# Performance work log

Hardware: AMD Instinct MI355X
Metric: run time of the kernel (lower is better)

Reference implementation:

```python
import jax, jax.numpy as jnp
import numpy as np

PATCH = 5
DIM = 256
HEADS = 8
EPS = 1e-5


def split_patches(t, p):
    # t: [B,H,W,C] -> overlapping patches [B,H,W,p,p,C], stride 1, zero-pad p//2
    pad = p // 2
    tp = jnp.pad(t, ((0, 0), (pad, pad), (pad, pad), (0, 0)))
    H, W = t.shape[1], t.shape[2]
    rows = jnp.arange(H)[:, None] + jnp.arange(p)[None, :]  # [H,p]
    cols = jnp.arange(W)[:, None] + jnp.arange(p)[None, :]  # [W,p]
    return tp[:, rows[:, None, :, None], cols[None, :, None, :], :]


def layernorm(v, g, b):
    mu = jnp.mean(v, axis=-1, keepdims=True)
    var = jnp.var(v, axis=-1, keepdims=True)
    return (v - mu) * jax.lax.rsqrt(var + EPS) * g + b


def mha(q, k, v, w, b, mask):
    # w: [4,D,D] stacked (Wq,Wk,Wv,Wo), b: [4,D]; q:[N,Lq,D], k,v:[N,Lk,D]
    N, Lq, D = q.shape
    dh = D // HEADS
    qh = (q @ w[0] + b[0]).reshape(N, Lq, HEADS, dh)
    kh = (k @ w[1] + b[1]).reshape(N, -1, HEADS, dh)
    vh = (v @ w[2] + b[2]).reshape(N, -1, HEADS, dh)
    sc = jnp.einsum('nqhd,nkhd->nhqk', qh, kh) * (1.0 / float(np.sqrt(dh)))
    if mask is not None:
        sc = jnp.where(mask, sc, jnp.asarray(-1e9, sc.dtype))
    a = jax.nn.softmax(sc, axis=-1)
    o = jnp.einsum('nhqk,nkhd->nqhd', a, vh).reshape(N, Lq, D)
    return o @ w[3] + b[3], a


def setup_inputs() -> dict:
    key = jax.random.key(0)
    ks = jax.random.split(key, 10)
    B, H, W, D = 1, 64, 64, DIM
    x = jax.random.normal(ks[0], (B, H, W, D), dtype=jnp.float32)
    memory = jax.random.normal(ks[1], (B, H, W, D), dtype=jnp.float32)
    active_nodes = jax.random.randint(ks[2], (B, H, W), 0, 2).astype(bool)
    s = 0.05
    return {
        'x': x, 'memory': memory, 'active_nodes': active_nodes,
        'attn_w': jax.random.normal(ks[3], (4, D, D), dtype=jnp.float32) * s,
        'attn_b': jnp.zeros((4, D), dtype=jnp.float32),
        'pattn_w': jax.random.normal(ks[4], (4, D, D), dtype=jnp.float32) * s,
        'pattn_b': jnp.zeros((4, D), dtype=jnp.float32),
        'ff_w1': jax.random.normal(ks[5], (D, 2 * D), dtype=jnp.float32) * s,
        'ff_b1': jnp.zeros((2 * D,), dtype=jnp.float32),
        'ff_w2': jax.random.normal(ks[6], (2 * D, D), dtype=jnp.float32) * s,
        'ff_b2': jnp.zeros((D,), dtype=jnp.float32),
        'ln_g': jnp.ones((3, D), dtype=jnp.float32),   # norm1, norm2, norm3
        'ln_b': jnp.zeros((3, D), dtype=jnp.float32),
    }


def reference(x, memory, active_nodes, attn_w, attn_b, pattn_w, pattn_b,
              ff_w1, ff_b1, ff_w2, ff_b2, ln_g, ln_b):
    B, H, W, D = x.shape
    p = PATCH
    center = p // 2
    L = p * p
    cp = L // 2  # flattened center point

    act = active_nodes[..., None]                      # [B,H,W,1] bool
    ap = split_patches(act, p)                         # [B,H,W,p,p,1]
    # faithful to source: zeroes the entire patch at GRID position (center,center)
    ap = ap.at[:, center, center].set(False)
    wo_center = jnp.any(ap.reshape(B, H, W, L, 1), axis=3)  # [B,H,W,1]
    act = jnp.logical_and(wo_center, act)
    ap = split_patches(act, p)                         # recomputed with updated mask

    xp = split_patches(x, p) * ap                      # zero inactive neighbors
    xp = xp.reshape(B, H, W, L, D)
    mp = split_patches(memory, p).reshape(B, H, W, L, D)
    mask = ap[..., 0].reshape(B, H, W, L)

    N = B * H * W
    keys = xp.reshape(N, L, D)
    mem = mp.reshape(N, L, D)
    q = keys[:, cp:cp + 1, :]                          # [N,1,D]
    m = mask.reshape(N, L)[:, None, None, :]           # [N,1,1,L]

    # EncoderLayer (eval mode: dropout = identity)
    s_, attn = mha(q, keys, keys, attn_w, attn_b, m)
    s = layernorm(q + s_, ln_g[0], ln_b[0])            # norm1
    s_, _ = mha(s, mem, mem, pattn_w, pattn_b, None)
    s = layernorm(s + s_, ln_g[2], ln_b[2])            # norm3
    ff = jax.nn.relu(s @ ff_w1 + ff_b1) @ ff_w2 + ff_b2
    s = layernorm(s + ff, ln_g[1], ln_b[1])            # norm2

    out = jnp.where(act, s[:, 0, :].reshape(B, H, W, D), jnp.asarray(0.0, x.dtype))
    return out, act[..., 0]
```

## Files before the change

kernel.cpp:

```cpp
#include <hip/hip_runtime.h>
#include <math.h>

#define D 256
#define H2 512
#define HEADS 8
#define L 25
#define GH 64
#define GW 64
#define NN 4096
#define EPS 1e-5f
#define SCALE 0.17677669529663687f
#define NND 1048576

typedef __attribute__((ext_vector_type(8))) short short8;
typedef __attribute__((ext_vector_type(4))) float f32x4;

__device__ __forceinline__ bool act_at(const int* __restrict__ active, int h, int w) {
    if (h < 0 || h >= GH || w < 0 || w >= GW) return false;
    if (h == 2 && w == 2) return false;
    return active[h * GW + w] != 0;
}

__device__ __forceinline__ unsigned short f2b(float f) {
    unsigned u = __float_as_uint(f);
    u += 0x7fffu + ((u >> 16) & 1u);
    return (unsigned short)(u >> 16);
}
__device__ __forceinline__ float b2f(short v) {
    return __uint_as_float(((unsigned)(unsigned short)v) << 16);
}

__global__ __launch_bounds__(256)
void prep_kernel(const float* __restrict__ x, const float* __restrict__ mem,
                 const int* __restrict__ active,
                 const float* __restrict__ attn_w, const float* __restrict__ pattn_w,
                 const float* __restrict__ ff_w1, const float* __restrict__ ff_w2,
                 const float* __restrict__ pattn_b,
                 unsigned short* __restrict__ xmB, unsigned short* __restrict__ memB,
                 unsigned short* __restrict__ wB,
                 unsigned short* __restrict__ k2bias, unsigned short* __restrict__ v2bias) {
    const int tid = threadIdx.x;
    const int bid = blockIdx.x;
    if (bid < 192) {
        __shared__ float tile[64][65];
        const float* src; unsigned short* dst;
        int i0, n0, srcLen, dstLen;
        if (bid < 128) {
            int mat = bid >> 4, t16 = bid & 15;
            i0 = (t16 >> 2) * 64; n0 = (t16 & 3) * 64;
            src = (mat < 4) ? (attn_w + mat * 65536) : (pattn_w + (mat - 4) * 65536);
            dst = wB + mat * 65536;
            srcLen = 256; dstLen = 256;
        } else if (bid < 160) {
            int t = bid - 128;
            i0 = (t >> 3) * 64; n0 = (t & 7) * 64;
            src = ff_w1; dst = wB + 524288;
            srcLen = 512; dstLen = 256;
        } else {
            int t = bid - 160;
            i0 = (t >> 2) * 64; n0 = (t & 3) * 64;
            src = ff_w2; dst = wB + 655360;
            srcLen = 256; dstLen = 512;
        }
        int c = tid & 63, r4 = tid >> 6;
        for (int rr = 0; rr < 64; rr += 4)
            tile[rr + r4][c] = src[(size_t)(i0 + rr + r4) * srcLen + n0 + c];
        __syncthreads();
        for (int rr = 0; rr < 64; rr += 4) {
            int r = rr + r4;
            dst[(size_t)(n0 + r) * dstLen + i0 + c] = f2b(tile[c][r]);
        }
    } else {
        const int t0 = (bid - 192) * 256 + tid;
        for (int t = t0; t < 524800; t += 512 * 256) {
            if (t < 262144) {
                int n = t >> 6;
                bool a = act_at(active, n >> 6, n & 63);
                float4 v = ((const float4*)x)[t];
                ushort4 u;
                u.x = f2b(a ? v.x : 0.0f); u.y = f2b(a ? v.y : 0.0f);
                u.z = f2b(a ? v.z : 0.0f); u.w = f2b(a ? v.w : 0.0f);
                ((ushort4*)xmB)[t] = u;
            } else if (t < 524288) {
                int tt = t - 262144;
                float4 v = ((const float4*)mem)[tt];
                ushort4 u;
                u.x = f2b(v.x); u.y = f2b(v.y); u.z = f2b(v.z); u.w = f2b(v.w);
                ((ushort4*)memB)[tt] = u;
            } else {
                int tt = t - 524288;
                if (tt < 256) k2bias[tt] = f2b(pattn_b[256 + tt]);
                else          v2bias[tt - 256] = f2b(pattn_b[512 + (tt - 256)]);
            }
        }
    }
}

__global__ __launch_bounds__(256)
void proj_gemm(const unsigned short* __restrict__ xmB,
               const unsigned short* __restrict__ memB,
               const unsigned short* __restrict__ wB,
               const float* __restrict__ attn_b, const float* __restrict__ pattn_b,
               unsigned short* __restrict__ q1b, unsigned short* __restrict__ k1b,
               unsigned short* __restrict__ v1b, unsigned short* __restrict__ k2b,
               unsigned short* __restrict__ v2b) {
    const int s  = blockIdx.y >> 2;
    const int n0 = (blockIdx.y & 3) * 64;
    const unsigned short* A  = (s < 3) ? xmB : memB;
    const int wtIdx = (s < 3) ? s : (s + 2);
    const unsigned short* WT = wB + (size_t)wtIdx * 65536;
    const float* bias = (s < 3) ? (attn_b + s * 256) : (pattn_b + (s - 2) * 256);
    unsigned short* outB;
    switch (s) { case 0: outB = q1b; break; case 1: outB = k1b; break;
                 case 2: outB = v1b; break; case 3: outB = k2b; break;
                 default: outB = v2b; }

    const int tid = threadIdx.x;
    const int wave = tid >> 6, lane = tid & 63;
    const int m0 = blockIdx.x * 64 + wave * 16;
    const int lr = lane & 15;
    const int lk = (lane >> 4) << 3;
    f32x4 acc[4] = {};
    const unsigned short* arow = A  + (size_t)(m0 + lr) * 256 + lk;
    const unsigned short* brow = WT + (size_t)(n0 + lr) * 256 + lk;
    #pragma unroll
    for (int kk = 0; kk < 256; kk += 32) {
        short8 a = *(const short8*)(arow + kk);
        #pragma unroll
        for (int nf = 0; nf < 4; ++nf) {
            short8 b = *(const short8*)(brow + (size_t)nf * 16 * 256 + kk);
            acc[nf] = __builtin_amdgcn_mfma_f32_16x16x32_bf16(a, b, acc[nf], 0, 0, 0);
        }
    }
    const int rbase = m0 + ((lane >> 4) << 2);
    #pragma unroll
    for (int nf = 0; nf < 4; ++nf) {
        int c = n0 + nf * 16 + lr;
        float bc = bias[c];
        #pragma unroll
        for (int jj = 0; jj < 4; ++jj)
            outB[(size_t)(rbase + jj) * 256 + c] = f2b(acc[nf][jj] + bc);
    }
}

#define KV_OFF   0
#define ACT_OFF  51200
#define WGT_OFF  51328
#define REDA_OFF 64128
#define REDB_OFF 64640
#define STAT_OFF 65152
#define SMEM_SZ  65280
#define T1B_OFF  0
#define SB_OFF   8448
#define HB_OFF   16896

__device__ __forceinline__ void load_union(const unsigned short* __restrict__ base,
                                           int h, int w0, int fallback,
                                           unsigned short (*kvU)[256], int tid) {
    for (int c = tid; c < 3200; c += 512) {
        int u = c >> 5, part = c & 31;
        int r = u / 20;
        int hh = h - 2 + r, ww = w0 - 2 + (u - r * 20);
        bool ib = ((unsigned)hh < GH) && ((unsigned)ww < GW);
        int row = ib ? ((hh << 6) | ww) : fallback;
        *(uint4*)&kvU[u][part * 8] = *(const uint4*)(base + (size_t)row * 256 + part * 8);
    }
}

__global__ __launch_bounds__(512)
void fused_kernel(const int* __restrict__ active, const float* __restrict__ x,
                  const unsigned short* __restrict__ wB,
                  const float* __restrict__ attn_b, const float* __restrict__ pattn_b,
                  const float* __restrict__ ff_b1, const float* __restrict__ ff_b2,
                  const float* __restrict__ ln_g, const float* __restrict__ ln_b,
                  const unsigned short* __restrict__ q1b,
                  const unsigned short* __restrict__ k1b,
                  const unsigned short* __restrict__ v1b,
                  const unsigned short* __restrict__ k2b,
                  const unsigned short* __restrict__ v2b,
                  float* __restrict__ out) {
    const int tid = threadIdx.x;
    const int wv = tid >> 6, lane = tid & 63;
    const int lr = lane & 15, qi = lane >> 4;
    const int bid = ((blockIdx.x & 7) << 5) | (blockIdx.x >> 3);
    const int n0 = bid * 16;
    const int h = n0 >> 6, w0 = n0 & 63;
    const int half = lane >> 5, lam = lane & 31;
    const int m = wv * 2 + half;

    __shared__ __align__(16) char smem[SMEM_SZ];
    unsigned short (*kvU)[256] = (unsigned short(*)[256])(smem + KV_OFF);
    unsigned char* actU        = (unsigned char*)(smem + ACT_OFF);
    float (*wgt)[8][25]        = (float(*)[8][25])(smem + WGT_OFF);
    float (*redA)[8]           = (float(*)[8])(smem + REDA_OFF);
    float (*redB)[8]           = (float(*)[8])(smem + REDB_OFF);
    float (*stats)[2]          = (float(*)[2])(smem + STAT_OFF);
    unsigned short (*T1b)[264] = (unsigned short(*)[264])(smem + T1B_OFF);
    unsigned short (*Sb)[264]  = (unsigned short(*)[264])(smem + SB_OFF);
    unsigned short (*Hb)[520]  = (unsigned short(*)[520])(smem + HB_OFF);

    if (tid < 100) {
        int r = tid / 20;
        int hh = h - 2 + r, ww = w0 - 2 + (tid - r * 20);
        actU[tid] = act_at(active, hh, ww) ? 1 : 0;
    }
    load_union(k1b, h, w0, 0, kvU, tid);
    __syncthreads();

    {
        float q[8];
        short8 qv = *(const short8*)(q1b + (size_t)(n0 + m) * 256 + lam * 8);
        #pragma unroll
        for (int j = 0; j < 8; ++j) q[j] = b2f(qv[j]);
        #pragma unroll 5
        for (int l = 0; l < L; ++l) {
            int u = (l / 5) * 20 + m + (l % 5);
            short8 kv = *(const short8*)&kvU[u][lam * 8];
            float p = q[0] * b2f(kv[0]);
            #pragma unroll
            for (int j = 1; j < 8; ++j) p = fmaf(q[j], b2f(kv[j]), p);
            p += __shfl_xor(p, 1); p += __shfl_xor(p, 2);
            float sv = actU[u] ? p * SCALE : -1e30f;
            if ((lam & 3) == 0) wgt[m][lam >> 2][l] = sv;
        }
    }
    __syncthreads();
    if (tid < 128) {
        int mm = tid >> 3, hd = tid & 7;
        float mx = -1e30f;
        for (int l = 0; l < L; ++l) mx = fmaxf(mx, wgt[mm][hd][l]);
        float sum = 0.0f;
        for (int l = 0; l < L; ++l) { float e = expf(wgt[mm][hd][l] - mx); wgt[mm][hd][l] = e; sum += e; }
        float inv = 1.0f / sum;
        for (int l = 0; l < L; ++l) wgt[mm][hd][l] *= inv;
    }
    __syncthreads();
    load_union(v1b, h, w0, 0, kvU, tid);
    __syncthreads();
    {
        float o[8] = {0.f,0.f,0.f,0.f,0.f,0.f,0.f,0.f};
        #pragma unroll 5
        for (int l = 0; l < L; ++l) {
            int u = (l / 5) * 20 + m + (l % 5);
            if (actU[u]) {
                float wt = wgt[m][lam >> 2][l];
                short8 v8 = *(const short8*)&kvU[u][lam * 8];
                #pragma unroll
                for (int j = 0; j < 8; ++j) o[j] = fmaf(wt, b2f(v8[j]), o[j]);
            }
        }
        __syncthreads();
        unsigned short u8[8];
        #pragma unroll
        for (int j = 0; j < 8; ++j) u8[j] = f2b(o[j]);
        *(uint4*)&T1b[m][lam * 8] = *(uint4*)u8;
    }
    __syncthreads();

    float sreg[2][4];
    {
        const unsigned short* Wo1T = wB + 3 * 65536;
        f32x4 acc[2] = {};
        #pragma unroll
        for (int kk = 0; kk < 256; kk += 32) {
            short8 a = *(const short8*)&T1b[lr][qi * 8 + kk];
            #pragma unroll
            for (int nf = 0; nf < 2; ++nf) {
                short8 b = *(const short8*)(Wo1T + (size_t)(wv * 32 + nf * 16 + lr) * 256 + qi * 8 + kk);
                acc[nf] = __builtin_amdgcn_mfma_f32_16x16x32_bf16(a, b, acc[nf], 0, 0, 0);
            }
        }
        float v[2][4], s1[4] = {0.f,0.f,0.f,0.f}, s2[4] = {0.f,0.f,0.f,0.f};
        #pragma unroll
        for (int nf = 0; nf < 2; ++nf) {
            int c = wv * 32 + nf * 16 + lr;
            float bc = attn_b[768 + c];
            #pragma unroll
            for (int jj = 0; jj < 4; ++jj) {
                int row = n0 + qi * 4 + jj;
                float vv = acc[nf][jj] + bc + x[(size_t)row * D + c];
                v[nf][jj] = vv; s1[jj] += vv; s2[jj] += vv * vv;
            }
        }
        #pragma unroll
        for (int jj = 0; jj < 4; ++jj) {
            #pragma unroll
            for (int off = 1; off < 16; off <<= 1) {
                s1[jj] += __shfl_xor(s1[jj], off);
                s2[jj] += __shfl_xor(s2[jj], off);
            }
        }
        if (lr == 0) {
            #pragma unroll
            for (int jj = 0; jj < 4; ++jj) { redA[qi*4+jj][wv] = s1[jj]; redB[qi*4+jj][wv] = s2[jj]; }
        }
        __syncthreads();
        if (tid < 16) {
            float a1 = 0.f, a2 = 0.f;
            #pragma unroll
            for (int q8 = 0; q8 < 8; ++q8) { a1 += redA[tid][q8]; a2 += redB[tid][q8]; }
            float mu = a1 * (1.0f / D);
            float var = a2 * (1.0f / D) - mu * mu;
            stats[tid][0] = mu; stats[tid][1] = rsqrtf(var + EPS);
        }
        __syncthreads();
        #pragma unroll
        for (int nf = 0; nf < 2; ++nf) {
            int c = wv * 32 + nf * 16 + lr;
            float gg = ln_g[c], bb = ln_b[c];
            #pragma unroll
            for (int jj = 0; jj < 4; ++jj) {
                int ridx = qi * 4 + jj;
                float ov = (v[nf][jj] - stats[ridx][0]) * stats[ridx][1] * gg + bb;
                sreg[nf][jj] = ov;
                Sb[ridx][c] = f2b(ov);
            }
        }
    }
    __syncthreads();

    {
        const unsigned short* Wq2T = wB + 4 * 65536;
        f32x4 acc[2] = {};
        #pragma unroll
        for (int kk = 0; kk < 256; kk += 32) {
            short8 a = *(const short8*)&Sb[lr][qi * 8 + kk];
            #pragma unroll
            for (int nf = 0; nf < 2; ++nf) {
                short8 b = *(const short8*)(Wq2T + (size_t)(wv * 32 + nf * 16 + lr) * 256 + qi * 8 + kk);
                acc[nf] = __builtin_amdgcn_mfma_f32_16x16x32_bf16(a, b, acc[nf], 0, 0, 0);
            }
        }
        __syncthreads();
        #pragma unroll
        for (int nf = 0; nf < 2; ++nf) {
            int c = wv * 32 + nf * 16 + lr;
            float bc = pattn_b[c];
            #pragma unroll
            for (int jj = 0; jj < 4; ++jj)
                T1b[qi * 4 + jj][c] = f2b(acc[nf][jj] + bc);
        }
    }
    __syncthreads();

    float q2[8];
    {
        short8 qv = *(const short8*)&T1b[m][lam * 8];
        #pragma unroll
        for (int j = 0; j < 8; ++j) q2[j] = b2f(qv[j]);
    }
    __syncthreads();
    load_union(k2b, h, w0, NN, kvU, tid);
    __syncthreads();

    #pragma unroll 5
    for (int l = 0; l < L; ++l) {
        int u = (l / 5) * 20 + m + (l % 5);
        short8 kv = *(const short8*)&kvU[u][lam * 8];
        float p = q2[0] * b2f(kv[0]);
        #pragma unroll
        for (int j = 1; j < 8; ++j) p = fmaf(q2[j], b2f(kv[j]), p);
        p += __shfl_xor(p, 1); p += __shfl_xor(p, 2);
        if ((lam & 3) == 0) wgt[m][lam >> 2][l] = p * SCALE;
    }
    __syncthreads();
    if (tid < 128) {
        int mm = tid >> 3, hd = tid & 7;
        float mx = -1e30f;
        for (int l = 0; l < L; ++l) mx = fmaxf(mx, wgt[mm][hd][l]);
        float sum = 0.0f;
        for (int l = 0; l < L; ++l) { float e = expf(wgt[mm][hd][l] - mx); wgt[mm][hd][l] = e; sum += e; }
        float inv = 1.0f / sum;
        for (int l = 0; l < L; ++l) wgt[mm][hd][l] *= inv;
    }
    __syncthreads();
    load_union(v2b, h, w0, NN, kvU, tid);
    __syncthreads();
    {
        float o[8] = {0.f,0.f,0.f,0.f,0.f,0.f,0.f,0.f};
        #pragma unroll 5
        for (int l = 0; l < L; ++l) {
            int u = (l / 5) * 20 + m + (l % 5);
            float wt = wgt[m][lam >> 2][l];
            short8 v8 = *(const short8*)&kvU[u][lam * 8];
            #pragma unroll
            for (int j = 0; j < 8; ++j) o[j] = fmaf(wt, b2f(v8[j]), o[j]);
        }
        __syncthreads();
        unsigned short u8[8];
        #pragma unroll
        for (int j = 0; j < 8; ++j) u8[j] = f2b(o[j]);
        *(uint4*)&T1b[m][lam * 8] = *(uint4*)u8;
    }
    __syncthreads();

    float s2reg[2][4];
    {
        const unsigned short* Wo2T = wB + 7 * 65536;
        f32x4 acc[2] = {};
        #pragma unroll
        for (int kk = 0; kk < 256; kk += 32) {
            short8 a = *(const short8*)&T1b[lr][qi * 8 + kk];
            #pragma unroll
            for (int nf = 0; nf < 2; ++nf) {
                short8 b = *(const short8*)(Wo2T + (size_t)(wv * 32 + nf * 16 + lr) * 256 + qi * 8 + kk);
                acc[nf] = __builtin_amdgcn_mfma_f32_16x16x32_bf16(a, b, acc[nf], 0, 0, 0);
            }
        }
        float v[2][4], s1[4] = {0.f,0.f,0.f,0.f}, s2[4] = {0.f,0.f,0.f,0.f};
        #pragma unroll
        for (int nf = 0; nf < 2; ++nf) {
            int c = wv * 32 + nf * 16 + lr;
            float bc = pattn_b[768 + c];
            #pragma unroll
            for (int jj = 0; jj < 4; ++jj) {
                float vv = acc[nf][jj] + bc + sreg[nf][jj];
                v[nf][jj] = vv; s1[jj] += vv; s2[jj] += vv * vv;
            }
        }
        #pragma unroll
        for (int jj = 0; jj < 4; ++jj) {
            #pragma unroll
            for (int off = 1; off < 16; off <<= 1) {
                s1[jj] += __shfl_xor(s1[jj], off);
                s2[jj] += __shfl_xor(s2[jj], off);
            }
        }
        if (lr == 0) {
            #pragma unroll
            for (int jj = 0; jj < 4; ++jj) { redA[qi*4+jj][wv] = s1[jj]; redB[qi*4+jj][wv] = s2[jj]; }
        }
        __syncthreads();
        if (tid < 16) {
            float a1 = 0.f, a2 = 0.f;
            #pragma unroll
            for (int q8 = 0; q8 < 8; ++q8) { a1 += redA[tid][q8]; a2 += redB[tid][q8]; }
            float mu = a1 * (1.0f / D);
            float var = a2 * (1.0f / D) - mu * mu;
            stats[tid][0] = mu; stats[tid][1] = rsqrtf(var + EPS);
        }
        __syncthreads();
        #pragma unroll
        for (int nf = 0; nf < 2; ++nf) {
            int c = wv * 32 + nf * 16 + lr;
            float gg = ln_g[512 + c], bb = ln_b[512 + c];
            #pragma unroll
            for (int jj = 0; jj < 4; ++jj) {
                int ridx = qi * 4 + jj;
                float ov = (v[nf][jj] - stats[ridx][0]) * stats[ridx][1] * gg + bb;
                s2reg[nf][jj] = ov;
                Sb[ridx][c] = f2b(ov);
            }
        }
    }
    __syncthreads();

    {
        const unsigned short* W1T = wB + 524288;
        f32x4 acc[4] = {};
        #pragma unroll
        for (int kk = 0; kk < 256; kk += 32) {
            short8 a = *(const short8*)&Sb[lr][qi * 8 + kk];
            #pragma unroll
            for (int nf = 0; nf < 4; ++nf) {
                short8 b = *(const short8*)(W1T + (size_t)(wv * 64 + nf * 16 + lr) * 256 + qi * 8 + kk);
                acc[nf] = __builtin_amdgcn_mfma_f32_16x16x32_bf16(a, b, acc[nf], 0, 0, 0);
            }
        }
        #pragma unroll
        for (int nf = 0; nf < 4; ++nf) {
            int c = wv * 64 + nf * 16 + lr;
            float bc = ff_b1[c];
            #pragma unroll
            for (int jj = 0; jj < 4; ++jj)
                Hb[qi * 4 + jj][c] = f2b(fmaxf(acc[nf][jj] + bc, 0.0f));
        }
    }
    __syncthreads();

    {
        const unsigned short* W2T = wB + 655360;
        f32x4 acc[2] = {};
        #pragma unroll
        for (int kk = 0; kk < 512; kk += 32) {
            short8 a = *(const short8*)&Hb[lr][qi * 8 + kk];
            #pragma unroll
            for (int nf = 0; nf < 2; ++nf) {
                short8 b = *(const short8*)(W2T + (size_t)(wv * 32 + nf * 16 + lr) * 512 + qi * 8 + kk);
                acc[nf] = __builtin_amdgcn_mfma_f32_16x16x32_bf16(a, b, acc[nf], 0, 0, 0);
            }
        }
        float v[2][4], s1[4] = {0.f,0.f,0.f,0.f}, s2[4] = {0.f,0.f,0.f,0.f};
        #pragma unroll
        for (int nf = 0; nf < 2; ++nf) {
            int c = wv * 32 + nf * 16 + lr;
            float bc = ff_b2[c];
            #pragma unroll
            for (int jj = 0; jj < 4; ++jj) {
                float vv = acc[nf][jj] + bc + s2reg[nf][jj];
                v[nf][jj] = vv; s1[jj] += vv; s2[jj] += vv * vv;
            }
        }
        #pragma unroll
        for (int jj = 0; jj < 4; ++jj) {
            #pragma unroll
            for (int off = 1; off < 16; off <<= 1) {
                s1[jj] += __shfl_xor(s1[jj], off);
                s2[jj] += __shfl_xor(s2[jj], off);
            }
        }
        if (lr == 0) {
            #pragma unroll
            for (int jj = 0; jj < 4; ++jj) { redA[qi*4+jj][wv] = s1[jj]; redB[qi*4+jj][wv] = s2[jj]; }
        }
        __syncthreads();
        if (tid < 16) {
            float a1 = 0.f, a2 = 0.f;
            #pragma unroll
            for (int q8 = 0; q8 < 8; ++q8) { a1 += redA[tid][q8]; a2 += redB[tid][q8]; }
            float mu = a1 * (1.0f / D);
            float var = a2 * (1.0f / D) - mu * mu;
            stats[tid][0] = mu; stats[tid][1] = rsqrtf(var + EPS);
        }
        __syncthreads();
        bool arow_act[4];
        #pragma unroll
        for (int jj = 0; jj < 4; ++jj) {
            int row = n0 + qi * 4 + jj;
            arow_act[jj] = act_at(active, row >> 6, row & 63);
        }
        #pragma unroll
        for (int nf = 0; nf < 2; ++nf) {
            int c = wv * 32 + nf * 16 + lr;
            float gg = ln_g[256 + c], bb = ln_b[256 + c];
            #pragma unroll
            for (int jj = 0; jj < 4; ++jj) {
                int ridx = qi * 4 + jj;
                float ov = (v[nf][jj] - stats[ridx][0]) * stats[ridx][1] * gg + bb;
                out[(size_t)(n0 + ridx) * D + c] = arow_act[jj] ? ov : 0.0f;
            }
        }
        if (tid < 16) {
            int row = n0 + tid;
            out[(size_t)NND + row] = act_at(active, row >> 6, row & 63) ? 1.0f : 0.0f;
        }
    }
}

extern "C" void kernel_launch(void* const* d_in, const int* in_sizes, int n_in,
                              void* d_out, int out_size, void* d_ws, size_t ws_size,
                              hipStream_t stream) {
    const float* x       = (const float*)d_in[0];
    const float* memory  = (const float*)d_in[1];
    const int*   active  = (const int*)d_in[2];
    const float* attn_w  = (const float*)d_in[3];
    const float* attn_b  = (const float*)d_in[4];
    const float* pattn_w = (const float*)d_in[5];
    const float* pattn_b = (const float*)d_in[6];
    const float* ff_w1   = (const float*)d_in[7];
    const float* ff_b1   = (const float*)d_in[8];
    const float* ff_w2   = (const float*)d_in[9];
    const float* ff_b2   = (const float*)d_in[10];
    const float* ln_g    = (const float*)d_in[11];
    const float* ln_b    = (const float*)d_in[12];
    float* out = (float*)d_out;

    unsigned short* wsb = (unsigned short*)d_ws;
    unsigned short* xmB  = wsb;
    unsigned short* memB = wsb + (size_t)NND;
    unsigned short* wB   = wsb + 2 * (size_t)NND;
    unsigned short* q1b  = wB + 786432;
    unsigned short* k1b  = q1b + (size_t)NND;
    unsigned short* v1b  = k1b + (size_t)NND;
    unsigned short* k2b  = v1b + (size_t)NND;
    unsigned short* v2b  = k2b + (size_t)NND + 256;

    hipLaunchKernelGGL(prep_kernel, dim3(704), dim3(256), 0, stream,
                       x, memory, active, attn_w, pattn_w, ff_w1, ff_w2, pattn_b,
                       xmB, memB, wB, k2b + (size_t)NND, v2b + (size_t)NND);
    hipLaunchKernelGGL(proj_gemm, dim3(64, 20), dim3(256), 0, stream,
                       xmB, memB, wB, attn_b, pattn_b, q1b, k1b, v1b, k2b, v2b);
    hipLaunchKernelGGL(fused_kernel, dim3(256), dim3(512), 0, stream,
                       active, x, wB, attn_b, pattn_b, ff_b1, ff_b2, ln_g, ln_b,
                       q1b, k1b, v1b, k2b, v2b, out);
}
```

Before: 91.11 us.

## Fuse input bf16 conversion into projection GEMM and double-buffer neighbor K/V loads

The prep kernel no longer converts x and memory to bf16 buffers. The projection GEMM now reads fp32 inputs directly, applies the active mask and converts in registers, which removes a full write and re-read of two activation tensors. The fused kernel now uses separate K and V LDS buffers in a larger dynamic shared allocation. It prefetches the next stage's K2/V2 union into registers while softmax and attention compute run, cutting several serialized global-load barriers. The trade-off is more LDS per block, about 150KB, and more registers. The GEMM also reads fp32 A twice from global, which is more traffic per tile than bf16.

```diff
diff --git a/kernel.cpp b/kernel.cpp
--- a/kernel.cpp
+++ b/kernel.cpp
@@ -31,12 +31,9 @@
 }
 
 __global__ __launch_bounds__(256)
-void prep_kernel(const float* __restrict__ x, const float* __restrict__ mem,
-                 const int* __restrict__ active,
-                 const float* __restrict__ attn_w, const float* __restrict__ pattn_w,
+void prep_kernel(const float* __restrict__ attn_w, const float* __restrict__ pattn_w,
                  const float* __restrict__ ff_w1, const float* __restrict__ ff_w2,
                  const float* __restrict__ pattn_b,
-                 unsigned short* __restrict__ xmB, unsigned short* __restrict__ memB,
                  unsigned short* __restrict__ wB,
                  unsigned short* __restrict__ k2bias, unsigned short* __restrict__ v2bias) {
     const int tid = threadIdx.x;
@@ -71,34 +68,16 @@
             dst[(size_t)(n0 + r) * dstLen + i0 + c] = f2b(tile[c][r]);
         }
     } else {
-        const int t0 = (bid - 192) * 256 + tid;
-        for (int t = t0; t < 524800; t += 512 * 256) {
-            if (t < 262144) {
-                int n = t >> 6;
-                bool a = act_at(active, n >> 6, n & 63);
-                float4 v = ((const float4*)x)[t];
-                ushort4 u;
-                u.x = f2b(a ? v.x : 0.0f); u.y = f2b(a ? v.y : 0.0f);
-                u.z = f2b(a ? v.z : 0.0f); u.w = f2b(a ? v.w : 0.0f);
-                ((ushort4*)xmB)[t] = u;
-            } else if (t < 524288) {
-                int tt = t - 262144;
-                float4 v = ((const float4*)mem)[tt];
-                ushort4 u;
-                u.x = f2b(v.x); u.y = f2b(v.y); u.z = f2b(v.z); u.w = f2b(v.w);
-                ((ushort4*)memB)[tt] = u;
-            } else {
-                int tt = t - 524288;
-                if (tt < 256) k2bias[tt] = f2b(pattn_b[256 + tt]);
-                else          v2bias[tt - 256] = f2b(pattn_b[512 + (tt - 256)]);
-            }
+        if (tid < 256) {
+            k2bias[tid] = f2b(pattn_b[256 + tid]);
+            v2bias[tid] = f2b(pattn_b[512 + tid]);
         }
     }
 }
 
 __global__ __launch_bounds__(256)
-void proj_gemm(const unsigned short* __restrict__ xmB,
-               const unsigned short* __restrict__ memB,
+void proj_gemm(const float* __restrict__ x, const float* __restrict__ mem,
+               const int* __restrict__ active,
                const unsigned short* __restrict__ wB,
                const float* __restrict__ attn_b, const float* __restrict__ pattn_b,
                unsigned short* __restrict__ q1b, unsigned short* __restrict__ k1b,
@@ -106,7 +85,8 @@
                unsigned short* __restrict__ v2b) {
     const int s  = blockIdx.y >> 2;
     const int n0 = (blockIdx.y & 3) * 64;
-    const unsigned short* A  = (s < 3) ? xmB : memB;
+    const float* Asrc = (s < 3) ? x : mem;
+    const bool useMask = (s < 3);
     const int wtIdx = (s < 3) ? s : (s + 2);
     const unsigned short* WT = wB + (size_t)wtIdx * 65536;
     const float* bias = (s < 3) ? (attn_b + s * 256) : (pattn_b + (s - 2) * 256);
@@ -120,12 +100,25 @@
     const int m0 = blockIdx.x * 64 + wave * 16;
     const int lr = lane & 15;
     const int lk = (lane >> 4) << 3;
+    const int arowIdx = m0 + lr;
+    const bool rowAct = !useMask || act_at(active, arowIdx >> 6, arowIdx & 63);
+
     f32x4 acc[4] = {};
-    const unsigned short* arow = A  + (size_t)(m0 + lr) * 256 + lk;
+    const float* arow = Asrc + (size_t)arowIdx * 256 + lk;
     const unsigned short* brow = WT + (size_t)(n0 + lr) * 256 + lk;
     #pragma unroll
     for (int kk = 0; kk < 256; kk += 32) {
-        short8 a = *(const short8*)(arow + kk);
+        float4 a0 = *(const float4*)(arow + kk);
+        float4 a1 = *(const float4*)(arow + kk + 4);
+        short8 a;
+        a[0] = rowAct ? (short)f2b(a0.x) : (short)0;
+        a[1] = rowAct ? (short)f2b(a0.y) : (short)0;
+        a[2] = rowAct ? (short)f2b(a0.z) : (short)0;
+        a[3] = rowAct ? (short)f2b(a0.w) : (short)0;
+        a[4] = rowAct ? (short)f2b(a1.x) : (short)0;
+        a[5] = rowAct ? (short)f2b(a1.y) : (short)0;
+        a[6] = rowAct ? (short)f2b(a1.z) : (short)0;
+        a[7] = rowAct ? (short)f2b(a1.w) : (short)0;
         #pragma unroll
         for (int nf = 0; nf < 4; ++nf) {
             short8 b = *(const short8*)(brow + (size_t)nf * 16 * 256 + kk);
@@ -143,27 +136,33 @@
     }
 }
 
-#define KV_OFF   0
-#define ACT_OFF  51200
-#define WGT_OFF  51328
-#define REDA_OFF 64128
-#define REDB_OFF 64640
-#define STAT_OFF 65152
-#define SMEM_SZ  65280
-#define T1B_OFF  0
-#define SB_OFF   8448
-#define HB_OFF   16896
-
-__device__ __forceinline__ void load_union(const unsigned short* __restrict__ base,
-                                           int h, int w0, int fallback,
-                                           unsigned short (*kvU)[256], int tid) {
+#define BK_OFF   0
+#define BV_OFF   51200
+#define WGT_OFF  102400
+#define T1B_OFF  115200
+#define SB_OFF   123648
+#define HB_OFF   132096
+#define ACT_OFF  148736
+#define REDA_OFF 148864
+#define REDB_OFF 149376
+#define STAT_OFF 149888
+#define SMEM_SZ  150016
+
+__device__ __forceinline__ int union_row(int c, int h, int w0, int fallback) {
+    int u = c >> 5;
+    int r = u / 20;
+    int hh = h - 2 + r, ww = w0 - 2 + (u - r * 20);
+    bool ib = ((unsigned)hh < GH) && ((unsigned)ww < GW);
+    return ib ? ((hh << 6) | ww) : fallback;
+}
+
+__device__ __forceinline__ void load_union_lds(const unsigned short* __restrict__ base,
+                                               int h, int w0, int fallback,
+                                               unsigned short (*dst)[256], int tid) {
     for (int c = tid; c < 3200; c += 512) {
+        int row = union_row(c, h, w0, fallback);
         int u = c >> 5, part = c & 31;
-        int r = u / 20;
-        int hh = h - 2 + r, ww = w0 - 2 + (u - r * 20);
-        bool ib = ((unsigned)hh < GH) && ((unsigned)ww < GW);
-        int row = ib ? ((hh << 6) | ww) : fallback;
-        *(uint4*)&kvU[u][part * 8] = *(const uint4*)(base + (size_t)row * 256 + part * 8);
+        *(uint4*)&dst[u][part * 8] = *(const uint4*)(base + (size_t)row * 256 + part * 8);
     }
 }
 
@@ -179,32 +178,34 @@
                   const unsigned short* __restrict__ k2b,
                   const unsigned short* __restrict__ v2b,
                   float* __restrict__ out) {
+    extern __shared__ __align__(16) char smem[];
+    unsigned short (*bufK)[256] = (unsigned short(*)[256])(smem + BK_OFF);
+    unsigned short (*bufV)[256] = (unsigned short(*)[256])(smem + BV_OFF);
+    float (*wgt)[8][25]         = (float(*)[8][25])(smem + WGT_OFF);
+    unsigned short (*T1b)[264]  = (unsigned short(*)[264])(smem + T1B_OFF);
+    unsigned short (*Sb)[264]   = (unsigned short(*)[264])(smem + SB_OFF);
+    unsigned short (*Hb)[520]   = (unsigned short(*)[520])(smem + HB_OFF);
+    unsigned char* actU         = (unsigned char*)(smem + ACT_OFF);
+    float (*redA)[8]            = (float(*)[8])(smem + REDA_OFF);
+    float (*redB)[8]            = (float(*)[8])(smem + REDB_OFF);
+    float (*stats)[2]           = (float(*)[2])(smem + STAT_OFF);
+
     const int tid = threadIdx.x;
     const int wv = tid >> 6, lane = tid & 63;
     const int lr = lane & 15, qi = lane >> 4;
+    const int half = lane >> 5, lam = lane & 31;
+    const int m = wv * 2 + half;
     const int bid = ((blockIdx.x & 7) << 5) | (blockIdx.x >> 3);
     const int n0 = bid * 16;
     const int h = n0 >> 6, w0 = n0 & 63;
-    const int half = lane >> 5, lam = lane & 31;
-    const int m = wv * 2 + half;
-
-    __shared__ __align__(16) char smem[SMEM_SZ];
-    unsigned short (*kvU)[256] = (unsigned short(*)[256])(smem + KV_OFF);
-    unsigned char* actU        = (unsigned char*)(smem + ACT_OFF);
-    float (*wgt)[8][25]        = (float(*)[8][25])(smem + WGT_OFF);
-    float (*redA)[8]           = (float(*)[8])(smem + REDA_OFF);
-    float (*redB)[8]           = (float(*)[8])(smem + REDB_OFF);
-    float (*stats)[2]          = (float(*)[2])(smem + STAT_OFF);
-    unsigned short (*T1b)[264] = (unsigned short(*)[264])(smem + T1B_OFF);
-    unsigned short (*Sb)[264]  = (unsigned short(*)[264])(smem + SB_OFF);
-    unsigned short (*Hb)[520]  = (unsigned short(*)[520])(smem + HB_OFF);
 
     if (tid < 100) {
         int r = tid / 20;
         int hh = h - 2 + r, ww = w0 - 2 + (tid - r * 20);
         actU[tid] = act_at(active, hh, ww) ? 1 : 0;
     }
-    load_union(k1b, h, w0, 0, kvU, tid);
+    load_union_lds(k1b, h, w0, 0, bufK, tid);
+    load_union_lds(v1b, h, w0, 0, bufV, tid);
     __syncthreads();
 
     {
@@ -215,7 +216,7 @@
         #pragma unroll 5
         for (int l = 0; l < L; ++l) {
             int u = (l / 5) * 20 + m + (l % 5);
-            short8 kv = *(const short8*)&kvU[u][lam * 8];
+            short8 kv = *(const short8*)&bufK[u][lam * 8];
             float p = q[0] * b2f(kv[0]);
             #pragma unroll
             for (int j = 1; j < 8; ++j) p = fmaf(q[j], b2f(kv[j]), p);
@@ -223,6 +224,167 @@
             float sv = actU[u] ? p * SCALE : -1e30f;
             if ((lam & 3) == 0) wgt[m][lam >> 2][l] = sv;
         }
+    }
+    __syncthreads();
+
+    uint4 pre[7];
+    {
+        #pragma unroll
+        for (int k = 0; k < 7; ++k) {
+            int c = tid + k * 512;
+            int cc = (c < 3200) ? c : 3199;
+            int row = union_row(cc, h, w0, NN);
+            pre[k] = *(const uint4*)(k2b + (size_t)row * 256 + (cc & 31) * 8);
+        }
+        if (tid < 128) {
+            int mm = tid >> 3, hd = tid & 7;
+            float mx = -1e30f;
+            for (int l = 0; l < L; ++l) mx = fmaxf(mx, wgt[mm][hd][l]);
+            float sum = 0.0f;
+            for (int l = 0; l < L; ++l) { float e = expf(wgt[mm][hd][l] - mx); wgt[mm][hd][l] = e; sum += e; }
+            float inv = 1.0f / sum;
+            for (int l = 0; l < L; ++l) wgt[mm][hd][l] *= inv;
+        }
+        #pragma unroll
+        for (int k = 0; k < 7; ++k) {
+            int c = tid + k * 512;
+            if (c < 3200)
+                *(uint4*)&bufK[c >> 5][(c & 31) * 8] = pre[k];
+        }
+    }
+    __syncthreads();
+
+    {
+        #pragma unroll
+        for (int k = 0; k < 7; ++k) {
+            int c = tid + k * 512;
+            int cc = (c < 3200) ? c : 3199;
+            int row = union_row(cc, h, w0, NN);
+            pre[k] = *(const uint4*)(v2b + (size_t)row * 256 + (cc & 31) * 8);
+        }
+        float o[8] = {0.f,0.f,0.f,0.f,0.f,0.f,0.f,0.f};
+        #pragma unroll 5
+        for (int l = 0; l < L; ++l) {
+            int u = (l / 5) * 20 + m + (l % 5);
+            if (actU[u]) {
+                float wt = wgt[m][lam >> 2][l];
+                short8 v8 = *(const short8*)&bufV[u][lam * 8];
+                #pragma unroll
+                for (int j = 0; j < 8; ++j) o[j] = fmaf(wt, b2f(v8[j]), o[j]);
+            }
+        }
+        unsigned short u8[8];
+        #pragma unroll
+        for (int j = 0; j < 8; ++j) u8[j] = f2b(o[j]);
+        *(uint4*)&T1b[m][lam * 8] = *(uint4*)u8;
+    }
+    __syncthreads();
+
+    float sreg[2][4];
+    {
+        #pragma unroll
+        for (int k = 0; k < 7; ++k) {
+            int c = tid + k * 512;
+            if (c < 3200)
+                *(uint4*)&bufV[c >> 5][(c & 31) * 8] = pre[k];
+        }
+        const unsigned short* Wo1T = wB + 3 * 65536;
+        f32x4 acc[2] = {};
+        #pragma unroll
+        for (int kk = 0; kk < 256; kk += 32) {
+            short8 a = *(const short8*)&T1b[lr][qi * 8 + kk];
+            #pragma unroll
+            for (int nf = 0; nf < 2; ++nf) {
+                short8 b = *(const short8*)(Wo1T + (size_t)(wv * 32 + nf * 16 + lr) * 256 + qi * 8 + kk);
+                acc[nf] = __builtin_amdgcn_mfma_f32_16x16x32_bf16(a, b, acc[nf], 0, 0, 0);
+            }
+        }
+        float v[2][4], s1[4] = {0.f,0.f,0.f,0.f}, s2[4] = {0.f,0.f,0.f,0.f};
+        #pragma unroll
+        for (int nf = 0; nf < 2; ++nf) {
+            int c = wv * 32 + nf * 16 + lr;
+            float bc = attn_b[768 + c];
+            #pragma unroll
+            for (int jj = 0; jj < 4; ++jj) {
+                int row = n0 + qi * 4 + jj;
+                float vv = acc[nf][jj] + bc + x[(size_t)row * D + c];
+                v[nf][jj] = vv; s1[jj] += vv; s2[jj] += vv * vv;
+            }
+        }
+        #pragma unroll
+        for (int jj = 0; jj < 4; ++jj) {
+            #pragma unroll
+            for (int off = 1; off < 16; off <<= 1) {
+                s1[jj] += __shfl_xor(s1[jj], off);
+                s2[jj] += __shfl_xor(s2[jj], off);
+            }
+        }
+        if (lr == 0) {
+            #pragma unroll
+            for (int jj = 0; jj < 4; ++jj) { redA[qi*4+jj][wv] = s1[jj]; redB[qi*4+jj][wv] = s2[jj]; }
+        }
+        __syncthreads();
+        if (tid < 16) {
+            float a1 = 0.f, a2 = 0.f;
+            #pragma unroll
+            for (int q8 = 0; q8 < 8; ++q8) { a1 += redA[tid][q8]; a2 += redB[tid][q8]; }
+            float mu = a1 * (1.0f / D);
+            float var = a2 * (1.0f / D) - mu * mu;
+            stats[tid][0] = mu; stats[tid][1] = rsqrtf(var + EPS);
+        }
+        __syncthreads();
+        #pragma unroll
+        for (int nf = 0; nf < 2; ++nf) {
+            int c = wv * 32 + nf * 16 + lr;
+            float gg = ln_g[c], bb = ln_b[c];
+            #pragma unroll
+            for (int jj = 0; jj < 4; ++jj) {
+                int ridx = qi * 4 + jj;
+                float ov = (v[nf][jj] - stats[ridx][0]) * stats[ridx][1] * gg + bb;
+                sreg[nf][jj] = ov;
+                Sb[ridx][c] = f2b(ov);
+            }
+        }
+    }
+    __syncthreads();
+
+    float q2[8];
+    {
+        const unsigned short* Wq2T = wB + 4 * 65536;
+        f32x4 acc[2] = {};
+        #pragma unroll
+        for (int kk = 0; kk < 256; kk += 32) {
+            short8 a = *(const short8*)&Sb[lr][qi * 8 + kk];
+            #pragma unroll
+            for (int nf = 0; nf < 2; ++nf) {
+                short8 b = *(const short8*)(Wq2T + (size_t)(wv * 32 + nf * 16 + lr) * 256 + qi * 8 + kk);
+                acc[nf] = __builtin_amdgcn_mfma_f32_16x16x32_bf16(a, b, acc[nf], 0, 0, 0);
+            }
+        }
+        __syncthreads();
+        #pragma unroll
+        for (int nf = 0; nf < 2; ++nf) {
+            int c = wv * 32 + nf * 16 + lr;
+            float bc = pattn_b[c];
+            #pragma unroll
+            for (int jj = 0; jj < 4; ++jj)
+                T1b[qi * 4 + jj][c] = f2b(acc[nf][jj] + bc);
+        }
+        __syncthreads();
+        short8 qv = *(const short8*)&T1b[m][lam * 8];
+        #pragma unroll
+        for (int j = 0; j < 8; ++j) q2[j] = b2f(qv[j]);
+    }
+
+    #pragma unroll 5
+    for (int l = 0; l < L; ++l) {
+        int u = (l / 5) * 20 + m + (l % 5);
+        short8 kv = *(const short8*)&bufK[u][lam * 8];
+        float p = q2[0] * b2f(kv[0]);
+        #pragma unroll
+        for (int j = 1; j < 8; ++j) p = fmaf(q2[j], b2f(kv[j]), p);
+        p += __shfl_xor(p, 1); p += __shfl_xor(p, 2);
+        if ((lam & 3) == 0) wgt[m][lam >> 2][l] = p * SCALE;
     }
     __syncthreads();
     if (tid < 128) {
@@ -235,158 +397,17 @@
         for (int l = 0; l < L; ++l) wgt[mm][hd][l] *= inv;
     }
     __syncthreads();
-    load_union(v1b, h, w0, 0, kvU, tid);
-    __syncthreads();
-    {
-        float o[8] = {0.f,0.f,0.f,0.f,0.f,0.f,0.f,0.f};
-        #pragma unroll 5
-        for (int l = 0; l < L; ++l) {
-            int u = (l / 5) * 20 + m + (l % 5);
-            if (actU[u]) {
-                float wt = wgt[m][lam >> 2][l];
-                short8 v8 = *(const short8*)&kvU[u][lam * 8];
-                #pragma unroll
-                for (int j = 0; j < 8; ++j) o[j] = fmaf(wt, b2f(v8[j]), o[j]);
-            }
-        }
-        __syncthreads();
-        unsigned short u8[8];
-        #pragma unroll
-        for (int j = 0; j < 8; ++j) u8[j] = f2b(o[j]);
-        *(uint4*)&T1b[m][lam * 8] = *(uint4*)u8;
-    }
-    __syncthreads();
-
-    float sreg[2][4];
-    {
-        const unsigned short* Wo1T = wB + 3 * 65536;
-        f32x4 acc[2] = {};
-        #pragma unroll
-        for (int kk = 0; kk < 256; kk += 32) {
-            short8 a = *(const short8*)&T1b[lr][qi * 8 + kk];
-            #pragma unroll
-            for (int nf = 0; nf < 2; ++nf) {
-                short8 b = *(const short8*)(Wo1T + (size_t)(wv * 32 + nf * 16 + lr) * 256 + qi * 8 + kk);
-                acc[nf] = __builtin_amdgcn_mfma_f32_16x16x32_bf16(a, b, acc[nf], 0, 0, 0);
-            }
-        }
-        float v[2][4], s1[4] = {0.f,0.f,0.f,0.f}, s2[4] = {0.f,0.f,0.f,0.f};
-        #pragma unroll
-        for (int nf = 0; nf < 2; ++nf) {
-            int c = wv * 32 + nf * 16 + lr;
-            float bc = attn_b[768 + c];
-            #pragma unroll
-            for (int jj = 0; jj < 4; ++jj) {
-                int row = n0 + qi * 4 + jj;
-                float vv = acc[nf][jj] + bc + x[(size_t)row * D + c];
-                v[nf][jj] = vv; s1[jj] += vv; s2[jj] += vv * vv;
-            }
-        }
-        #pragma unroll
-        for (int jj = 0; jj < 4; ++jj) {
-            #pragma unroll
-            for (int off = 1; off < 16; off <<= 1) {
-                s1[jj] += __shfl_xor(s1[jj], off);
-                s2[jj] += __shfl_xor(s2[jj], off);
-            }
-        }
-        if (lr == 0) {
-            #pragma unroll
-            for (int jj = 0; jj < 4; ++jj) { redA[qi*4+jj][wv] = s1[jj]; redB[qi*4+jj][wv] = s2[jj]; }
-        }
-        __syncthreads();
-        if (tid < 16) {
-            float a1 = 0.f, a2 = 0.f;
-            #pragma unroll
-            for (int q8 = 0; q8 < 8; ++q8) { a1 += redA[tid][q8]; a2 += redB[tid][q8]; }
-            float mu = a1 * (1.0f / D);
-            float var = a2 * (1.0f / D) - mu * mu;
-            stats[tid][0] = mu; stats[tid][1] = rsqrtf(var + EPS);
-        }
-        __syncthreads();
-        #pragma unroll
-        for (int nf = 0; nf < 2; ++nf) {
-            int c = wv * 32 + nf * 16 + lr;
-            float gg = ln_g[c], bb = ln_b[c];
-            #pragma unroll
-            for (int jj = 0; jj < 4; ++jj) {
-                int ridx = qi * 4 + jj;
-                float ov = (v[nf][jj] - stats[ridx][0]) * stats[ridx][1] * gg + bb;
-                sreg[nf][jj] = ov;
-                Sb[ridx][c] = f2b(ov);
-            }
-        }
-    }
-    __syncthreads();
-
-    {
-        const unsigned short* Wq2T = wB + 4 * 65536;
-        f32x4 acc[2] = {};
-        #pragma unroll
-        for (int kk = 0; kk < 256; kk += 32) {
-            short8 a = *(const short8*)&Sb[lr][qi * 8 + kk];
-            #pragma unroll
-            for (int nf = 0; nf < 2; ++nf) {
-                short8 b = *(const short8*)(Wq2T + (size_t)(wv * 32 + nf * 16 + lr) * 256 + qi * 8 + kk);
-                acc[nf] = __builtin_amdgcn_mfma_f32_16x16x32_bf16(a, b, acc[nf], 0, 0, 0);
-            }
-        }
-        __syncthreads();
-        #pragma unroll
-        for (int nf = 0; nf < 2; ++nf) {
-            int c = wv * 32 + nf * 16 + lr;
-            float bc = pattn_b[c];
-            #pragma unroll
-            for (int jj = 0; jj < 4; ++jj)
-                T1b[qi * 4 + jj][c] = f2b(acc[nf][jj] + bc);
-        }
-    }
-    __syncthreads();
-
-    float q2[8];
-    {
-        short8 qv = *(const short8*)&T1b[m][lam * 8];
-        #pragma unroll
-        for (int j = 0; j < 8; ++j) q2[j] = b2f(qv[j]);
-    }
-    __syncthreads();
-    load_union(k2b, h, w0, NN, kvU, tid);
-    __syncthreads();
-
-    #pragma unroll 5
-    for (int l = 0; l < L; ++l) {
-        int u = (l / 5) * 20 + m + (l % 5);
-        short8 kv = *(const short8*)&kvU[u][lam * 8];
-        float p = q2[0] * b2f(kv[0]);
-        #pragma unroll
-        for (int j = 1; j < 8; ++j) p = fmaf(q2[j], b2f(kv[j]), p);
-        p += __shfl_xor(p, 1); p += __shfl_xor(p, 2);
-        if ((lam & 3) == 0) wgt[m][lam >> 2][l] = p * SCALE;
-    }
-    __syncthreads();
-    if (tid < 128) {
-        int mm = tid >> 3, hd = tid & 7;
-        float mx = -1e30f;
-        for (int l = 0; l < L; ++l) mx = fmaxf(mx, wgt[mm][hd][l]);
-        float sum = 0.0f;
-        for (int l = 0; l < L; ++l) { float e = expf(wgt[mm][hd][l] - mx); wgt[mm][hd][l] = e; sum += e; }
-        float inv = 1.0f / sum;
-        for (int l = 0; l < L; ++l) wgt[mm][hd][l] *= inv;
-    }
-    __syncthreads();
-    load_union(v2b, h, w0, NN, kvU, tid);
-    __syncthreads();
+
     {
         float o[8] = {0.f,0.f,0.f,0.f,0.f,0.f,0.f,0.f};
         #pragma unroll 5
         for (int l = 0; l < L; ++l) {
             int u = (l / 5) * 20 + m + (l % 5);
             float wt = wgt[m][lam >> 2][l];
-            short8 v8 = *(const short8*)&kvU[u][lam * 8];
+            short8 v8 = *(const short8*)&bufV[u][lam * 8];
             #pragma unroll
             for (int j = 0; j < 8; ++j) o[j] = fmaf(wt, b2f(v8[j]), o[j]);
         }
-        __syncthreads();
         unsigned short u8[8];
         #pragma unroll
         for (int j = 0; j < 8; ++j) u8[j] = f2b(o[j]);
@@ -566,21 +587,27 @@
     float* out = (float*)d_out;
 
     unsigned short* wsb = (unsigned short*)d_ws;
-    unsigned short* xmB  = wsb;
-    unsigned short* memB = wsb + (size_t)NND;
-    unsigned short* wB   = wsb + 2 * (size_t)NND;
+    unsigned short* wB   = wsb;
     unsigned short* q1b  = wB + 786432;
     unsigned short* k1b  = q1b + (size_t)NND;
     unsigned short* v1b  = k1b + (size_t)NND;
     unsigned short* k2b  = v1b + (size_t)NND;
     unsigned short* v2b  = k2b + (size_t)NND + 256;
 
-    hipLaunchKernelGGL(prep_kernel, dim3(704), dim3(256), 0, stream,
-                       x, memory, active, attn_w, pattn_w, ff_w1, ff_w2, pattn_b,
-                       xmB, memB, wB, k2b + (size_t)NND, v2b + (size_t)NND);
+    static int attr_set = 0;
+    if (!attr_set) {
+        hipFuncSetAttribute(reinterpret_cast<const void*>(fused_kernel),
+                            hipFuncAttributeMaxDynamicSharedMemorySize, SMEM_SZ);
+        attr_set = 1;
+    }
+
+    hipLaunchKernelGGL(prep_kernel, dim3(193), dim3(256), 0, stream,
+                       attn_w, pattn_w, ff_w1, ff_w2, pattn_b,
+                       wB, k2b + (size_t)NND, v2b + (size_t)NND);
     hipLaunchKernelGGL(proj_gemm, dim3(64, 20), dim3(256), 0, stream,
-                       xmB, memB, wB, attn_b, pattn_b, q1b, k1b, v1b, k2b, v2b);
-    hipLaunchKernelGGL(fused_kernel, dim3(256), dim3(512), 0, stream,
+                       x, memory, active, wB, attn_b, pattn_b,
+                       q1b, k1b, v1b, k2b, v2b);
+    hipLaunchKernelGGL(fused_kernel, dim3(256), dim3(512), SMEM_SZ, stream,
                        active, x, wB, attn_b, pattn_b, ff_b1, ff_b2, ln_g, ln_b,
                        q1b, k1b, v1b, k2b, v2b, out);
 }
```

Result: slower. 102.2 us (+12.1%).

## Prefetch K/V neighbor unions into separate LDS buffers via async global-to-LDS DMA

Applied to the files above, without the earlier changes.

Replaces the synchronous register-staged load_union with global_load_lds DMA into separate K and V LDS buffers. K1 and V1 are loaded together up front. K2 is prefetched during the first softmax, and V2 during the first output projection. This overlaps the gather latency with compute and removes several barriers. LDS use grows to about 150KB through dynamic shared memory, and correctness depends on the barriers waiting for the DMA to complete.

```diff
diff --git a/kernel.cpp b/kernel.cpp
--- a/kernel.cpp
+++ b/kernel.cpp
@@ -28,6 +28,12 @@
 }
 __device__ __forceinline__ float b2f(short v) {
     return __uint_as_float(((unsigned)(unsigned short)v) << 16);
+}
+
+__device__ __forceinline__ void dma16(const unsigned short* g, unsigned short* l) {
+    __builtin_amdgcn_global_load_lds(
+        (const __attribute__((address_space(1))) unsigned int*)g,
+        (__attribute__((address_space(3))) unsigned int*)l, 16, 0, 0);
 }
 
 __global__ __launch_bounds__(256)
@@ -143,27 +149,36 @@
     }
 }
 
-#define KV_OFF   0
-#define ACT_OFF  51200
-#define WGT_OFF  51328
-#define REDA_OFF 64128
-#define REDB_OFF 64640
-#define STAT_OFF 65152
-#define SMEM_SZ  65280
-#define T1B_OFF  0
-#define SB_OFF   8448
-#define HB_OFF   16896
-
-__device__ __forceinline__ void load_union(const unsigned short* __restrict__ base,
-                                           int h, int w0, int fallback,
-                                           unsigned short (*kvU)[256], int tid) {
-    for (int c = tid; c < 3200; c += 512) {
-        int u = c >> 5, part = c & 31;
-        int r = u / 20;
-        int hh = h - 2 + r, ww = w0 - 2 + (u - r * 20);
-        bool ib = ((unsigned)hh < GH) && ((unsigned)ww < GW);
-        int row = ib ? ((hh << 6) | ww) : fallback;
-        *(uint4*)&kvU[u][part * 8] = *(const uint4*)(base + (size_t)row * 256 + part * 8);
+#define BK_OFF   0
+#define BV_OFF   51200
+#define WGT_OFF  102400
+#define T1B_OFF  115200
+#define SB_OFF   123648
+#define HB_OFF   132096
+#define ACT_OFF  148736
+#define REDA_OFF 148864
+#define REDB_OFF 149376
+#define STAT_OFF 149888
+#define SMEM_SZ  150016
+
+__device__ __forceinline__ int union_row(int c, int h, int w0, int fallback) {
+    int u = c >> 5;
+    int r = u / 20;
+    int hh = h - 2 + r, ww = w0 - 2 + (u - r * 20);
+    bool ib = ((unsigned)hh < GH) && ((unsigned)ww < GW);
+    return ib ? ((hh << 6) | ww) : fallback;
+}
+
+__device__ __forceinline__ void dma_union(const unsigned short* __restrict__ base,
+                                          int h, int w0, int fallback,
+                                          unsigned short* dstLds, int tid) {
+    #pragma unroll
+    for (int k = 0; k < 7; ++k) {
+        int c = tid + k * 512;
+        if (c < 3200) {
+            int row = union_row(c, h, w0, fallback);
+            dma16(base + (size_t)row * 256 + (c & 31) * 8, dstLds + (size_t)c * 8);
+        }
     }
 }
 
@@ -179,32 +194,34 @@
                   const unsigned short* __restrict__ k2b,
                   const unsigned short* __restrict__ v2b,
                   float* __restrict__ out) {
+    extern __shared__ __align__(16) char smem[];
+    unsigned short (*bufK)[256] = (unsigned short(*)[256])(smem + BK_OFF);
+    unsigned short (*bufV)[256] = (unsigned short(*)[256])(smem + BV_OFF);
+    float (*wgt)[8][25]         = (float(*)[8][25])(smem + WGT_OFF);
+    unsigned short (*T1b)[264]  = (unsigned short(*)[264])(smem + T1B_OFF);
+    unsigned short (*Sb)[264]   = (unsigned short(*)[264])(smem + SB_OFF);
+    unsigned short (*Hb)[520]   = (unsigned short(*)[520])(smem + HB_OFF);
+    unsigned char* actU         = (unsigned char*)(smem + ACT_OFF);
+    float (*redA)[8]            = (float(*)[8])(smem + REDA_OFF);
+    float (*redB)[8]            = (float(*)[8])(smem + REDB_OFF);
+    float (*stats)[2]           = (float(*)[2])(smem + STAT_OFF);
+
     const int tid = threadIdx.x;
     const int wv = tid >> 6, lane = tid & 63;
     const int lr = lane & 15, qi = lane >> 4;
+    const int half = lane >> 5, lam = lane & 31;
+    const int m = wv * 2 + half;
     const int bid = ((blockIdx.x & 7) << 5) | (blockIdx.x >> 3);
     const int n0 = bid * 16;
     const int h = n0 >> 6, w0 = n0 & 63;
-    const int half = lane >> 5, lam = lane & 31;
-    const int m = wv * 2 + half;
-
-    __shared__ __align__(16) char smem[SMEM_SZ];
-    unsigned short (*kvU)[256] = (unsigned short(*)[256])(smem + KV_OFF);
-    unsigned char* actU        = (unsigned char*)(smem + ACT_OFF);
-    float (*wgt)[8][25]        = (float(*)[8][25])(smem + WGT_OFF);
-    float (*redA)[8]           = (float(*)[8])(smem + REDA_OFF);
-    float (*redB)[8]           = (float(*)[8])(smem + REDB_OFF);
-    float (*stats)[2]          = (float(*)[2])(smem + STAT_OFF);
-    unsigned short (*T1b)[264] = (unsigned short(*)[264])(smem + T1B_OFF);
-    unsigned short (*Sb)[264]  = (unsigned short(*)[264])(smem + SB_OFF);
-    unsigned short (*Hb)[520]  = (unsigned short(*)[520])(smem + HB_OFF);
-
+
+    dma_union(k1b, h, w0, 0, (unsigned short*)(smem + BK_OFF), tid);
+    dma_union(v1b, h, w0, 0, (unsigned short*)(smem + BV_OFF), tid);
     if (tid < 100) {
         int r = tid / 20;
         int hh = h - 2 + r, ww = w0 - 2 + (tid - r * 20);
         actU[tid] = act_at(active, hh, ww) ? 1 : 0;
     }
-    load_union(k1b, h, w0, 0, kvU, tid);
     __syncthreads();
 
     {
@@ -215,7 +232,7 @@
         #pragma unroll 5
         for (int l = 0; l < L; ++l) {
             int u = (l / 5) * 20 + m + (l % 5);
-            short8 kv = *(const short8*)&kvU[u][lam * 8];
+            short8 kv = *(const short8*)&bufK[u][lam * 8];
             float p = q[0] * b2f(kv[0]);
             #pragma unroll
             for (int j = 1; j < 8; ++j) p = fmaf(q[j], b2f(kv[j]), p);
@@ -225,6 +242,8 @@
         }
     }
     __syncthreads();
+
+    dma_union(k2b, h, w0, NN, (unsigned short*)(smem + BK_OFF), tid);
     if (tid < 128) {
         int mm = tid >> 3, hd = tid & 7;
         float mx = -1e30f;
@@ -235,8 +254,7 @@
         for (int l = 0; l < L; ++l) wgt[mm][hd][l] *= inv;
     }
     __syncthreads();
-    load_union(v1b, h, w0, 0, kvU, tid);
-    __syncthreads();
+
     {
         float o[8] = {0.f,0.f,0.f,0.f,0.f,0.f,0.f,0.f};
         #pragma unroll 5
@@ -244,12 +262,11 @@
             int u = (l / 5) * 20 + m + (l % 5);
             if (actU[u]) {
                 float wt = wgt[m][lam >> 2][l];
-                short8 v8 = *(const short8*)&kvU[u][lam * 8];
+                short8 v8 = *(const short8*)&bufV[u][lam * 8];
                 #pragma unroll
                 for (int j = 0; j < 8; ++j) o[j] = fmaf(wt, b2f(v8[j]), o[j]);
             }
         }
-        __syncthreads();
         unsigned short u8[8];
         #pragma unroll
         for (int j = 0; j < 8; ++j) u8[j] = f2b(o[j]);
@@ -259,6 +276,7 @@
 
     float sreg[2][4];
     {
+        dma_union(v2b, h, w0, NN, (unsigned short*)(smem + BV_OFF), tid);
         const unsigned short* Wo1T = wB + 3 * 65536;
         f32x4 acc[2] = {};
         #pragma unroll
@@ -319,6 +337,7 @@
     }
     __syncthreads();
 
+    float q2[8];
     {
         const unsigned short* Wq2T = wB + 4 * 65536;
         f32x4 acc[2] = {};
@@ -331,7 +350,6 @@
                 acc[nf] = __builtin_amdgcn_mfma_f32_16x16x32_bf16(a, b, acc[nf], 0, 0, 0);
             }
         }
-        __syncthreads();
         #pragma unroll
         for (int nf = 0; nf < 2; ++nf) {
             int c = wv * 32 + nf * 16 + lr;
@@ -340,23 +358,16 @@
             for (int jj = 0; jj < 4; ++jj)
                 T1b[qi * 4 + jj][c] = f2b(acc[nf][jj] + bc);
         }
-    }
-    __syncthreads();
-
-    float q2[8];
-    {
+        __syncthreads();
         short8 qv = *(const short8*)&T1b[m][lam * 8];
         #pragma unroll
         for (int j = 0; j < 8; ++j) q2[j] = b2f(qv[j]);
     }
-    __syncthreads();
-    load_union(k2b, h, w0, NN, kvU, tid);
-    __syncthreads();
 
     #pragma unroll 5
     for (int l = 0; l < L; ++l) {
         int u = (l / 5) * 20 + m + (l % 5);
-        short8 kv = *(const short8*)&kvU[u][lam * 8];
+        short8 kv = *(const short8*)&bufK[u][lam * 8];
         float p = q2[0] * b2f(kv[0]);
         #pragma unroll
         for (int j = 1; j < 8; ++j) p = fmaf(q2[j], b2f(kv[j]), p);
@@ -374,19 +385,17 @@
         for (int l = 0; l < L; ++l) wgt[mm][hd][l] *= inv;
     }
     __syncthreads();
-    load_union(v2b, h, w0, NN, kvU, tid);
-    __syncthreads();
+
     {
         float o[8] = {0.f,0.f,0.f,0.f,0.f,0.f,0.f,0.f};
         #pragma unroll 5
         for (int l = 0; l < L; ++l) {
             int u = (l / 5) * 20 + m + (l % 5);
             float wt = wgt[m][lam >> 2][l];
-            short8 v8 = *(const short8*)&kvU[u][lam * 8];
+            short8 v8 = *(const short8*)&bufV[u][lam * 8];
             #pragma unroll
             for (int j = 0; j < 8; ++j) o[j] = fmaf(wt, b2f(v8[j]), o[j]);
         }
-        __syncthreads();
         unsigned short u8[8];
         #pragma unroll
         for (int j = 0; j < 8; ++j) u8[j] = f2b(o[j]);
@@ -575,12 +584,15 @@
     unsigned short* k2b  = v1b + (size_t)NND;
     unsigned short* v2b  = k2b + (size_t)NND + 256;
 
+    hipFuncSetAttribute(reinterpret_cast<const void*>(fused_kernel),
+                        hipFuncAttributeMaxDynamicSharedMemorySize, SMEM_SZ);
+
     hipLaunchKernelGGL(prep_kernel, dim3(704), dim3(256), 0, stream,
                        x, memory, active, attn_w, pattn_w, ff_w1, ff_w2, pattn_b,
                        xmB, memB, wB, k2b + (size_t)NND, v2b + (size_t)NND);
     hipLaunchKernelGGL(proj_gemm, dim3(64, 20), dim3(256), 0, stream,
                        xmB, memB, wB, attn_b, pattn_b, q1b, k1b, v1b, k2b, v2b);
-    hipLaunchKernelGGL(fused_kernel, dim3(256), dim3(512), 0, stream,
+    hipLaunchKernelGGL(fused_kernel, dim3(256), dim3(512), SMEM_SZ, stream,
                        active, x, wB, attn_b, pattn_b, ff_b1, ff_b2, ln_g, ln_b,
                        q1b, k1b, v1b, k2b, v2b, out);
 }
```

Result: no change. 89.63 us (-1.6%).
